# Performance work log

Hardware: AMD Instinct MI355X
Metric: run time of the kernel (lower is better)

Reference implementation:

```python
import jax, jax.numpy as jnp
import numpy as np

N_BITS_W = 8      # weight quant bits
N_BITS_A = 8      # activation quant bits
SCALE_RANGE_IN = 1.0
BN_EPS = 1e-5
ACT_THRES = 6.0   # ReLUN clamp


def _fake_quant(v, n_bits, scaling_range):
    """Symmetric uniform fake-quantization with straight-through estimator.
    Layer-wise scale from the max-abs value (Qmodes.layer_wise)."""
    qp = float(2 ** (n_bits - 1) - 1)
    alpha = scaling_range * jnp.max(jnp.abs(v))
    step = alpha / qp
    q = jnp.clip(jnp.round(v / step), -qp, qp) * step
    # STE: forward uses q, gradient flows through v unchanged
    return v + jax.lax.stop_gradient(q - v)


def setup_inputs() -> dict:
    key = jax.random.key(0)
    k1, k2 = jax.random.split(key)
    x = jax.random.normal(k1, (32, 16, 224, 224), dtype=jnp.float32)
    # Kaiming-ish scale for a 3x3 conv with 16 in-channels
    weight = jax.random.normal(k2, (16, 16, 3, 3), dtype=jnp.float32) * (1.0 / np.sqrt(16 * 9))
    gamma = jnp.ones((16,), dtype=jnp.float32)
    beta = jnp.zeros((16,), dtype=jnp.float32)
    return {"x": x, "weight": weight, "gamma": gamma, "beta": beta}


def reference(x, weight, gamma, beta):
    # --- GemmConv2d with quant_flag=True, noise_flag=False ---
    xq = _fake_quant(x, N_BITS_A, SCALE_RANGE_IN)
    wq = _fake_quant(weight, N_BITS_W, 1.0)
    y = jax.lax.conv_general_dilated(
        xq, wq,
        window_strides=(1, 1),
        padding=[(1, 1), (1, 1)],
        dimension_numbers=("NCHW", "OIHW", "NCHW"),
    )  # [N, Cout, H, W]
    # --- BatchNorm2d (training mode: batch statistics, biased variance) ---
    mean = jnp.mean(y, axis=(0, 2, 3))
    var = jnp.var(y, axis=(0, 2, 3))
    inv = gamma * jax.lax.rsqrt(var + BN_EPS)
    y = y * inv[None, :, None, None] + (beta - mean * inv)[None, :, None, None]
    # --- ReLUN(6): clamp to [0, act_thres] ---
    return jnp.clip(y, 0.0, ACT_THRES)
```

## Files before the change

kernel.cpp:

```cpp
#include <hip/hip_runtime.h>
#include <stdint.h>

#define QP 127.0f
#define HW2 50176
#define NPIX 1605632
#define NELEM 25690112
#define ABS_GRID 2048
#define NRG 56
#define NBLK_CONV 1792

#define WS_WQ    256
#define WS_SSUM  2560
#define WS_QSUM  2688
#define WS_BMAX  4096
#define WS_XQ    (1 << 20)

typedef int v4i __attribute__((ext_vector_type(4)));

__device__ __forceinline__ void stage_strip(const int4* __restrict__ xq,
                                            int4* sXs, int n, int r0, int tid) {
  #pragma unroll
  for (int j = 0; j < 6; ++j) {
    int g = r0 - 1 + j;
    if (tid < 224) {
      int4 v = {0, 0, 0, 0};
      if ((unsigned)g < 224u) v = xq[(n * 224 + g) * 224 + tid];
      sXs[j * 226 + 1 + tid] = v;
    } else if (tid < 226) {
      int4 z = {0, 0, 0, 0};
      sXs[j * 226 + ((tid == 224) ? 0 : 225)] = z;
    }
  }
}

__device__ __forceinline__ void conv_lane_setup(const int4* __restrict__ wq4,
                                                int ccol, int chunk,
                                                v4i (&bfrag)[3], int (&abase)[3]) {
  #pragma unroll
  for (int m = 0; m < 3; ++m) {
    int tap = 4 * m + chunk;
    v4i bv = {0, 0, 0, 0};
    if (tap <= 8) {
      int4 t = wq4[ccol * 9 + tap];
      bv[0] = t.x; bv[1] = t.y; bv[2] = t.z; bv[3] = t.w;
    }
    bfrag[m] = bv;
    int tc = (tap > 8) ? 8 : tap;
    int kh = tc / 3, kw = tc - kh * 3;
    abase[m] = kh * 226 + ccol + kw;
  }
}

__global__ __launch_bounds__(256) void k_absmax_wq(const float* __restrict__ x,
                                                   const float* __restrict__ w,
                                                   char* __restrict__ ws) {
  __shared__ float red[4];
  __shared__ float s_sw;
  float* hdr_f = (float*)ws;
  float* bmax = (float*)(ws + WS_BMAX);
  int* wq = (int*)(ws + WS_WQ);
  const int tid = threadIdx.x;

  if (blockIdx.x == 0 && tid < 16) {
    ((unsigned long long*)(ws + WS_SSUM))[tid] = 0ull;
    ((double*)(ws + WS_QSUM))[tid] = 0.0;
  }

  const float4* x4 = (const float4*)x;
  float m = 0.0f;
  for (int i = blockIdx.x * 256 + tid; i < NELEM / 4; i += ABS_GRID * 256) {
    float4 v = x4[i];
    m = fmaxf(m, fmaxf(fmaxf(fabsf(v.x), fabsf(v.y)),
                       fmaxf(fabsf(v.z), fabsf(v.w))));
  }
  #pragma unroll
  for (int off = 32; off; off >>= 1) m = fmaxf(m, __shfl_down(m, off, 64));
  if ((tid & 63) == 0) red[tid >> 6] = m;
  __syncthreads();
  if (tid == 0)
    bmax[blockIdx.x] = fmaxf(fmaxf(red[0], red[1]), fmaxf(red[2], red[3]));

  if (blockIdx.x == 0) {
    __syncthreads();
    float mw = 0.0f;
    for (int i = tid; i < 2304; i += 256) mw = fmaxf(mw, fabsf(w[i]));
    #pragma unroll
    for (int off = 32; off; off >>= 1) mw = fmaxf(mw, __shfl_down(mw, off, 64));
    if ((tid & 63) == 0) red[tid >> 6] = mw;
    __syncthreads();
    if (tid == 0) {
      float sw = fmaxf(fmaxf(red[0], red[1]), fmaxf(red[2], red[3])) / QP;
      hdr_f[1] = sw;
      s_sw = sw;
    }
    __syncthreads();
    float sw = s_sw;
    for (int i = tid; i < 576; i += 256) {
      int cout = i / 36; int r = i - cout * 36;
      int tap = r >> 2;  int c4 = r & 3;
      int kh = tap / 3, kw = tap - kh * 3;
      unsigned bits = 0;
      #pragma unroll
      for (int j = 0; j < 4; ++j) {
        int cin = c4 * 4 + j;
        float v = w[((cout * 16 + cin) * 3 + kh) * 3 + kw];
        int q = (int)rintf(v / sw);
        q = max(-127, min(127, q));
        bits |= ((unsigned)(q & 0xff)) << (8 * j);
      }
      wq[i] = (int)bits;
    }
  }
}

__global__ __launch_bounds__(256) void k_quant_stats(const float* __restrict__ x,
                                                     char* __restrict__ ws) {
  __shared__ int4 sXs[6 * 226];
  __shared__ int   sS[4][16];
  __shared__ float sQ[4][16];
  __shared__ float sRed4[4];
  const float* __restrict__ bmax = (const float*)(ws + WS_BMAX);
  const int4* __restrict__ wq4 = (const int4*)(ws + WS_WQ);
  float* hdr_f = (float*)ws;
  int4* xq = (int4*)(ws + WS_XQ);
  const int tid = threadIdx.x;

  float m = 0.0f;
  for (int i = tid; i < ABS_GRID; i += 256) m = fmaxf(m, bmax[i]);
  #pragma unroll
  for (int off = 32; off; off >>= 1) m = fmaxf(m, __shfl_down(m, off, 64));
  if ((tid & 63) == 0) sRed4[tid >> 6] = m;
  __syncthreads();
  const float sx =
      fmaxf(fmaxf(sRed4[0], sRed4[1]), fmaxf(sRed4[2], sRed4[3])) / QP;
  if (blockIdx.x == 0 && tid == 0) hdr_f[2] = sx;

  const int b = blockIdx.x;
  const int n = b / NRG, rg = b - n * NRG;
  const int r0 = rg * 4;

  for (int task = tid; task < 336; task += 256) {
    int j = task / 56, g = task - j * 56;
    int gr = r0 - 1 + j;
    int4 v[4] = {{0,0,0,0}, {0,0,0,0}, {0,0,0,0}, {0,0,0,0}};
    if ((unsigned)gr < 224u) {
      const float4* xb = (const float4*)x + (size_t)n * 16 * (HW2 / 4)
                         + gr * 56 + g;
      unsigned comp[4][4];
      #pragma unroll
      for (int k = 0; k < 4; ++k)
        #pragma unroll
        for (int q4 = 0; q4 < 4; ++q4) comp[k][q4] = 0u;
      #pragma unroll
      for (int c = 0; c < 16; ++c) {
        float4 vc = xb[c * (HW2 / 4)];
        float f[4] = {vc.x, vc.y, vc.z, vc.w};
        #pragma unroll
        for (int k = 0; k < 4; ++k) {
          int q = (int)rintf(f[k] / sx);
          q = max(-127, min(127, q));
          comp[k][c >> 2] |= ((unsigned)(q & 0xff)) << (8 * (c & 3));
        }
      }
      #pragma unroll
      for (int k = 0; k < 4; ++k) {
        v[k].x = (int)comp[k][0]; v[k].y = (int)comp[k][1];
        v[k].z = (int)comp[k][2]; v[k].w = (int)comp[k][3];
      }
      if (j >= 1 && j <= 4) {
        #pragma unroll
        for (int k = 0; k < 4; ++k)
          xq[(n * 224 + gr) * 224 + 4 * g + k] = v[k];
      }
    }
    #pragma unroll
    for (int k = 0; k < 4; ++k) sXs[j * 226 + 1 + 4 * g + k] = v[k];
  }
  if (tid >= 244) {
    int idx = tid - 244;
    int4 z = {0, 0, 0, 0};
    sXs[(idx >> 1) * 226 + ((idx & 1) ? 225 : 0)] = z;
  }

  const int lane = tid & 63, wid = tid >> 6;
  const int ccol = lane & 15, chunk = lane >> 4;
  v4i bfrag[3];
  int abase[3];
  conv_lane_setup(wq4, ccol, chunk, bfrag, abase);
  __syncthreads();

  int   sAcc = 0;
  float qAcc = 0.0f;
  for (int t = wid; t < 56; t += 4) {
    int ty = t / 14, x0 = (t - ty * 14) << 4;
    int off = ty * 226 + x0;
    v4i acc = {0, 0, 0, 0};
    #pragma unroll
    for (int m3 = 0; m3 < 3; ++m3) {
      int4 av = sXs[off + abase[m3]];
      v4i a; a[0] = av.x; a[1] = av.y; a[2] = av.z; a[3] = av.w;
      acc = __builtin_amdgcn_mfma_i32_16x16x64_i8(a, bfrag[m3], acc, 0, 0, 0);
    }
    #pragma unroll
    for (int r = 0; r < 4; ++r) {
      int d = acc[r];
      sAcc += d;
      float f = (float)d;
      qAcc += f * f;
    }
  }
  sAcc += __shfl_xor(sAcc, 16, 64);
  sAcc += __shfl_xor(sAcc, 32, 64);
  qAcc += __shfl_xor(qAcc, 16, 64);
  qAcc += __shfl_xor(qAcc, 32, 64);
  if (lane < 16) { sS[wid][ccol] = sAcc; sQ[wid][ccol] = qAcc; }
  __syncthreads();
  if (tid < 16) {
    int c = tid;
    long long s4 = (long long)sS[0][c] + sS[1][c] + sS[2][c] + sS[3][c];
    atomicAdd(((unsigned long long*)(ws + WS_SSUM)) + c,
              (unsigned long long)s4);
  } else if (tid < 32) {
    int c = tid & 15;
    float q4 = sQ[0][c] + sQ[1][c] + sQ[2][c] + sQ[3][c];
    atomicAdd(((double*)(ws + WS_QSUM)) + c, (double)q4);
  }
}

__global__ __launch_bounds__(256) void k_conv_out(const char* __restrict__ ws,
                                                  const float* __restrict__ gamma,
                                                  const float* __restrict__ beta,
                                                  float* __restrict__ out) {
  __shared__ int4 sXs[6 * 226];
  __shared__ float sAB[32];
  const int4* __restrict__ xq = (const int4*)(ws + WS_XQ);
  const int4* __restrict__ wq4 = (const int4*)(ws + WS_WQ);
  const float* hdr_f = (const float*)ws;

  const int tid = threadIdx.x;
  const int b = blockIdx.x;
  const int n = b / NRG, rg = b - n * NRG;
  const int r0 = rg * 4;

  stage_strip(xq, sXs, n, r0, tid);

  if (tid < 16) {
    unsigned long long us = ((const unsigned long long*)(ws + WS_SSUM))[tid];
    double S = (double)(long long)us;
    double Q = ((const double*)(ws + WS_QSUM))[tid];
    float sf = hdr_f[2] * hdr_f[1];
    double s = (double)sf;
    const double M = (double)NPIX;
    double mean = s * S / M;
    double ey2 = s * s * Q / M;
    double var = ey2 - mean * mean;
    double inv = (double)gamma[tid] / sqrt(var + 1e-5);
    sAB[tid] = (float)(s * inv);
    sAB[16 + tid] = (float)((double)beta[tid] - mean * inv);
  }

  const int lane = tid & 63, wid = tid >> 6;
  const int ccol = lane & 15, chunk = lane >> 4;
  v4i bfrag[3];
  int abase[3];
  conv_lane_setup(wq4, ccol, chunk, bfrag, abase);
  __syncthreads();

  const float Af = sAB[ccol];
  const float Bf = sAB[16 + ccol];

  float* oplane = out + ((size_t)n * 16 + ccol) * HW2;
  for (int t = wid; t < 56; t += 4) {
    int ty = t / 14, x0 = (t - ty * 14) << 4;
    int off = ty * 226 + x0;
    v4i acc = {0, 0, 0, 0};
    #pragma unroll
    for (int m3 = 0; m3 < 3; ++m3) {
      int4 av = sXs[off + abase[m3]];
      v4i a; a[0] = av.x; a[1] = av.y; a[2] = av.z; a[3] = av.w;
      acc = __builtin_amdgcn_mfma_i32_16x16x64_i8(a, bfrag[m3], acc, 0, 0, 0);
    }
    float4 o;
    o.x = fminf(fmaxf(fmaf((float)acc[0], Af, Bf), 0.0f), 6.0f);
    o.y = fminf(fmaxf(fmaf((float)acc[1], Af, Bf), 0.0f), 6.0f);
    o.z = fminf(fmaxf(fmaf((float)acc[2], Af, Bf), 0.0f), 6.0f);
    o.w = fminf(fmaxf(fmaf((float)acc[3], Af, Bf), 0.0f), 6.0f);
    int y = r0 + ty, xb = x0 + chunk * 4;
    *(float4*)&oplane[y * 224 + xb] = o;
  }
}

extern "C" void kernel_launch(void* const* d_in, const int* in_sizes, int n_in,
                              void* d_out, int out_size, void* d_ws, size_t ws_size,
                              hipStream_t stream) {
  const float* x = (const float*)d_in[0];
  const float* w = (const float*)d_in[1];
  const float* gamma = (const float*)d_in[2];
  const float* beta = (const float*)d_in[3];
  float* out = (float*)d_out;
  char* ws = (char*)d_ws;

  k_absmax_wq<<<ABS_GRID, 256, 0, stream>>>(x, w, ws);
  k_quant_stats<<<NBLK_CONV, 256, 0, stream>>>(x, ws);
  k_conv_out<<<NBLK_CONV, 256, 0, stream>>>(ws, gamma, beta, out);
}
```

Before: 276.0 us.

## Split quantization into its own pass and enlarge conv row strips to eight

Quantization of x moves out of the fused quant+stats kernel into a standalone elementwise kernel that writes the int8 packed tensor once. A new stats kernel re-reads that packed tensor from the workspace. Both conv kernels now process 8-row strips with a 10-row halo instead of 4-row strips with a 6-row halo, which halves the block count and cuts redundant halo loads. In exchange there is an extra kernel launch and an extra round trip of the quantized tensor through memory, but no halo rows are quantized twice.

```diff
diff --git a/kernel.cpp b/kernel.cpp
--- a/kernel.cpp
+++ b/kernel.cpp
@@ -6,8 +6,8 @@
 #define NPIX 1605632
 #define NELEM 25690112
 #define ABS_GRID 2048
-#define NRG 56
-#define NBLK_CONV 1792
+#define NRG8 28
+#define NBLK_CONV 896
 
 #define WS_WQ    256
 #define WS_SSUM  2560
@@ -17,10 +17,10 @@
 
 typedef int v4i __attribute__((ext_vector_type(4)));
 
-__device__ __forceinline__ void stage_strip(const int4* __restrict__ xq,
-                                            int4* sXs, int n, int r0, int tid) {
-  #pragma unroll
-  for (int j = 0; j < 6; ++j) {
+__device__ __forceinline__ void stage_strip10(const int4* __restrict__ xq,
+                                              int4* sXs, int n, int r0, int tid) {
+  #pragma unroll
+  for (int j = 0; j < 10; ++j) {
     int g = r0 - 1 + j;
     if (tid < 224) {
       int4 v = {0, 0, 0, 0};
@@ -113,14 +113,10 @@
   }
 }
 
-__global__ __launch_bounds__(256) void k_quant_stats(const float* __restrict__ x,
-                                                     char* __restrict__ ws) {
-  __shared__ int4 sXs[6 * 226];
-  __shared__ int   sS[4][16];
-  __shared__ float sQ[4][16];
+__global__ __launch_bounds__(256) void k_quant_x(const float* __restrict__ x,
+                                                 char* __restrict__ ws) {
   __shared__ float sRed4[4];
   const float* __restrict__ bmax = (const float*)(ws + WS_BMAX);
-  const int4* __restrict__ wq4 = (const int4*)(ws + WS_WQ);
   float* hdr_f = (float*)ws;
   int4* xq = (int4*)(ws + WS_XQ);
   const int tid = threadIdx.x;
@@ -135,52 +131,50 @@
       fmaxf(fmaxf(sRed4[0], sRed4[1]), fmaxf(sRed4[2], sRed4[3])) / QP;
   if (blockIdx.x == 0 && tid == 0) hdr_f[2] = sx;
 
+  int t = blockIdx.x * 256 + tid;
+  int p0 = t * 4;
+  int n = p0 / HW2;
+  int hw = p0 - n * HW2;
+  const float4* xb = (const float4*)(x + (size_t)n * 16 * HW2 + hw);
+  unsigned comp[4][4];
+  #pragma unroll
+  for (int j = 0; j < 4; ++j)
+    #pragma unroll
+    for (int k = 0; k < 4; ++k) comp[j][k] = 0u;
+  #pragma unroll
+  for (int c = 0; c < 16; ++c) {
+    float4 vc = xb[c * (HW2 / 4)];
+    float f[4] = {vc.x, vc.y, vc.z, vc.w};
+    #pragma unroll
+    for (int j = 0; j < 4; ++j) {
+      int q = (int)rintf(f[j] / sx);
+      q = max(-127, min(127, q));
+      comp[j][c >> 2] |= ((unsigned)(q & 0xff)) << (8 * (c & 3));
+    }
+  }
+  #pragma unroll
+  for (int j = 0; j < 4; ++j) {
+    int4 v;
+    v.x = (int)comp[j][0]; v.y = (int)comp[j][1];
+    v.z = (int)comp[j][2]; v.w = (int)comp[j][3];
+    xq[p0 + j] = v;
+  }
+}
+
+__global__ __launch_bounds__(256) void k_conv_stats(const char* __restrict__ ws_c,
+                                                    char* __restrict__ ws) {
+  __shared__ int4 sXs[10 * 226];
+  __shared__ int   sS[4][16];
+  __shared__ float sQ[4][16];
+  const int4* __restrict__ xq = (const int4*)(ws_c + WS_XQ);
+  const int4* __restrict__ wq4 = (const int4*)(ws_c + WS_WQ);
+
+  const int tid = threadIdx.x;
   const int b = blockIdx.x;
-  const int n = b / NRG, rg = b - n * NRG;
-  const int r0 = rg * 4;
-
-  for (int task = tid; task < 336; task += 256) {
-    int j = task / 56, g = task - j * 56;
-    int gr = r0 - 1 + j;
-    int4 v[4] = {{0,0,0,0}, {0,0,0,0}, {0,0,0,0}, {0,0,0,0}};
-    if ((unsigned)gr < 224u) {
-      const float4* xb = (const float4*)x + (size_t)n * 16 * (HW2 / 4)
-                         + gr * 56 + g;
-      unsigned comp[4][4];
-      #pragma unroll
-      for (int k = 0; k < 4; ++k)
-        #pragma unroll
-        for (int q4 = 0; q4 < 4; ++q4) comp[k][q4] = 0u;
-      #pragma unroll
-      for (int c = 0; c < 16; ++c) {
-        float4 vc = xb[c * (HW2 / 4)];
-        float f[4] = {vc.x, vc.y, vc.z, vc.w};
-        #pragma unroll
-        for (int k = 0; k < 4; ++k) {
-          int q = (int)rintf(f[k] / sx);
-          q = max(-127, min(127, q));
-          comp[k][c >> 2] |= ((unsigned)(q & 0xff)) << (8 * (c & 3));
-        }
-      }
-      #pragma unroll
-      for (int k = 0; k < 4; ++k) {
-        v[k].x = (int)comp[k][0]; v[k].y = (int)comp[k][1];
-        v[k].z = (int)comp[k][2]; v[k].w = (int)comp[k][3];
-      }
-      if (j >= 1 && j <= 4) {
-        #pragma unroll
-        for (int k = 0; k < 4; ++k)
-          xq[(n * 224 + gr) * 224 + 4 * g + k] = v[k];
-      }
-    }
-    #pragma unroll
-    for (int k = 0; k < 4; ++k) sXs[j * 226 + 1 + 4 * g + k] = v[k];
-  }
-  if (tid >= 244) {
-    int idx = tid - 244;
-    int4 z = {0, 0, 0, 0};
-    sXs[(idx >> 1) * 226 + ((idx & 1) ? 225 : 0)] = z;
-  }
+  const int n = b / NRG8, rg = b - n * NRG8;
+  const int r0 = rg * 8;
+
+  stage_strip10(xq, sXs, n, r0, tid);
 
   const int lane = tid & 63, wid = tid >> 6;
   const int ccol = lane & 15, chunk = lane >> 4;
@@ -191,7 +185,7 @@
 
   int   sAcc = 0;
   float qAcc = 0.0f;
-  for (int t = wid; t < 56; t += 4) {
+  for (int t = wid; t < 112; t += 4) {
     int ty = t / 14, x0 = (t - ty * 14) << 4;
     int off = ty * 226 + x0;
     v4i acc = {0, 0, 0, 0};
@@ -231,7 +225,7 @@
                                                   const float* __restrict__ gamma,
                                                   const float* __restrict__ beta,
                                                   float* __restrict__ out) {
-  __shared__ int4 sXs[6 * 226];
+  __shared__ int4 sXs[10 * 226];
   __shared__ float sAB[32];
   const int4* __restrict__ xq = (const int4*)(ws + WS_XQ);
   const int4* __restrict__ wq4 = (const int4*)(ws + WS_WQ);
@@ -239,10 +233,10 @@
 
   const int tid = threadIdx.x;
   const int b = blockIdx.x;
-  const int n = b / NRG, rg = b - n * NRG;
-  const int r0 = rg * 4;
-
-  stage_strip(xq, sXs, n, r0, tid);
+  const int n = b / NRG8, rg = b - n * NRG8;
+  const int r0 = rg * 8;
+
+  stage_strip10(xq, sXs, n, r0, tid);
 
   if (tid < 16) {
     unsigned long long us = ((const unsigned long long*)(ws + WS_SSUM))[tid];
@@ -270,7 +264,7 @@
   const float Bf = sAB[16 + ccol];
 
   float* oplane = out + ((size_t)n * 16 + ccol) * HW2;
-  for (int t = wid; t < 56; t += 4) {
+  for (int t = wid; t < 112; t += 4) {
     int ty = t / 14, x0 = (t - ty * 14) << 4;
     int off = ty * 226 + x0;
     v4i acc = {0, 0, 0, 0};
@@ -301,6 +295,7 @@
   char* ws = (char*)d_ws;
 
   k_absmax_wq<<<ABS_GRID, 256, 0, stream>>>(x, w, ws);
-  k_quant_stats<<<NBLK_CONV, 256, 0, stream>>>(x, ws);
+  k_quant_x<<<1568, 256, 0, stream>>>(x, ws);
+  k_conv_stats<<<NBLK_CONV, 256, 0, stream>>>(ws, ws);
   k_conv_out<<<NBLK_CONV, 256, 0, stream>>>(ws, gamma, beta, out);
 }
```

After: 249.4 us. -9.6%, faster.
